# Kernel tuning notes

Measured on AMD Instinct MI355X. Metric: run time of the kernel, lower is better.

## Reference

```python
import jax, jax.numpy as jnp
import numpy as np

NUM_HEADS = 16


def setup_inputs() -> dict:
    key = jax.random.key(0)
    k1, k2, k3 = jax.random.split(key, 3)
    B, S, D = 2, 2048, 1024
    x = jax.random.normal(k1, (B, S, D), dtype=jnp.float32)
    # qkv_bias=False -> no bias on qkv projection; output Dense has default bias
    w_qkv = jax.random.normal(k2, (D, 3 * D), dtype=jnp.float32) * (1.0 / np.sqrt(D))
    w_out = jax.random.normal(k3, (D, D), dtype=jnp.float32) * (1.0 / np.sqrt(D))
    b_out = jnp.zeros((D,), dtype=jnp.float32)
    return {"x": x, "w_qkv": w_qkv, "w_out": w_out, "b_out": b_out}


def reference(x, w_qkv, w_out, b_out):
    B, S, D = x.shape
    H = NUM_HEADS
    Dh = D // H
    scale = 1.0 / np.sqrt(Dh).astype(np.float32)

    qkv = jnp.einsum('bsd,de->bse', x, w_qkv)           # [B,S,3D]
    q, k, v = jnp.split(qkv, 3, axis=-1)
    split = lambda t: t.reshape(B, S, H, Dh).transpose(0, 2, 1, 3)  # [B,H,S,Dh]
    q, k, v = split(q), split(k), split(v)

    attn = jnp.einsum('bhid,bhjd->bhij', q, k) * scale  # [B,H,S,S]
    # mask=None -> all-ones mask combined with causal mask => causal float mask
    causal = jnp.tril(jnp.ones((S, S), dtype=jnp.float32))[None, None]
    attn = causal * attn + (1.0 - causal) * (-1e9)
    attn = jax.nn.softmax(attn, axis=-1)

    out = jnp.einsum('bhij,bhjd->bhid', attn, v)        # [B,H,S,Dh]
    out = out.transpose(0, 2, 1, 3).reshape(B, S, D)    # merge heads
    return jnp.einsum('bsd,de->bse', out, w_out) + b_out
```

## Files before the change

### kernel.cpp

```cpp
#include <hip/hip_runtime.h>

typedef unsigned short u16;
typedef __bf16 bf16x8 __attribute__((ext_vector_type(8)));
typedef unsigned short u16x8 __attribute__((ext_vector_type(8)));
typedef float f32x4 __attribute__((ext_vector_type(4)));

union Frag { u16x8 u; bf16x8 b; };

__device__ __forceinline__ u16 f2bf(float f) {
  unsigned u = __builtin_bit_cast(unsigned, f);
  u += 0x7fff + ((u >> 16) & 1);
  return (u16)(u >> 16);
}

__device__ __forceinline__ f32x4 mfma16(bf16x8 a, bf16x8 b, f32x4 c) {
  return __builtin_amdgcn_mfma_f32_16x16x32_bf16(a, b, c, 0, 0, 0);
}

typedef const __attribute__((address_space(1))) void* as1cv;
typedef __attribute__((address_space(3))) void* as3v;

__device__ __forceinline__ void glds16(const u16* g, u16* l) {
  __builtin_amdgcn_global_load_lds((as1cv)g, (as3v)l, 16, 0, 0);
}

__global__ __launch_bounds__(256) void castf_bf(const float* __restrict__ src,
                                                u16* __restrict__ dst, int n4) {
  int i = blockIdx.x * blockDim.x + threadIdx.x;
  int stride = gridDim.x * blockDim.x;
  for (; i < n4; i += stride) {
    float4 v = ((const float4*)src)[i];
    ushort4 o;
    o.x = f2bf(v.x); o.y = f2bf(v.y); o.z = f2bf(v.z); o.w = f2bf(v.w);
    ((ushort4*)dst)[i] = o;
  }
}

__global__ __launch_bounds__(256) void cast_transpose(const float* __restrict__ src,
                                                      u16* __restrict__ dst, int K, int N) {
  __shared__ float tile[32][33];
  int tn = N >> 5;
  int bk = blockIdx.x / tn, bn = blockIdx.x % tn;
  int k0 = bk << 5, n0 = bn << 5;
  int tx = threadIdx.x, ty = threadIdx.y;
#pragma unroll
  for (int i = 0; i < 4; i++)
    tile[ty + 8 * i][tx] = src[(size_t)(k0 + ty + 8 * i) * N + n0 + tx];
  __syncthreads();
#pragma unroll
  for (int i = 0; i < 4; i++)
    dst[(size_t)(n0 + ty + 8 * i) * K + k0 + tx] = f2bf(tile[tx][ty + 8 * i]);
}

template <int FP32OUT>
__global__ __launch_bounds__(256) void gemm_bt(const u16* __restrict__ A,
                                               const u16* __restrict__ BT,
                                               void* __restrict__ Cout,
                                               const float* __restrict__ bias,
                                               int N, int K, int nbc) {
  __shared__ u16 Al[128 * 32];
  __shared__ u16 Bl[128 * 32];
  int bid = blockIdx.x;
  int br = bid / nbc, bc = bid % nbc;
  int tid = threadIdx.x;
  int w = tid >> 6, l = tid & 63;
  int lg = l >> 4, lq = l & 15;
  int wr = w >> 1, wc = w & 1;

  f32x4 acc[4][4];
#pragma unroll
  for (int m = 0; m < 4; m++)
#pragma unroll
    for (int n = 0; n < 4; n++)
      acc[m][n] = (f32x4){0.f, 0.f, 0.f, 0.f};

  const u16* Ab = A + (size_t)(br * 128 + 32 * w + (l >> 2)) * K + (l & 3) * 8;
  const u16* Bb = BT + (size_t)(bc * 128 + 32 * w + (l >> 2)) * K + (l & 3) * 8;
  u16* Ald = Al + 32 * w * 32;
  u16* Bld = Bl + 32 * w * 32;

  for (int kt = 0; kt < K; kt += 32) {
    glds16(Ab + kt, Ald);
    glds16(Ab + (size_t)16 * K + kt, Ald + 16 * 32);
    glds16(Bb + kt, Bld);
    glds16(Bb + (size_t)16 * K + kt, Bld + 16 * 32);
    __syncthreads();

    Frag af[4], bf[4];
#pragma unroll
    for (int m = 0; m < 4; m++)
      af[m].u = *(const u16x8*)(Al + (64 * wr + 16 * m + lq) * 32 + lg * 8);
#pragma unroll
    for (int n = 0; n < 4; n++)
      bf[n].u = *(const u16x8*)(Bl + (64 * wc + 16 * n + lq) * 32 + lg * 8);
#pragma unroll
    for (int m = 0; m < 4; m++)
#pragma unroll
      for (int n = 0; n < 4; n++)
        acc[m][n] = mfma16(af[m].b, bf[n].b, acc[m][n]);
    __syncthreads();
  }

  int row0 = br * 128 + 64 * wr + lg * 4;
  int col0 = bc * 128 + 64 * wc + lq;
  if (FP32OUT) {
    float* C = (float*)Cout;
#pragma unroll
    for (int n = 0; n < 4; n++) {
      float bv = bias[col0 + 16 * n];
#pragma unroll
      for (int m = 0; m < 4; m++)
#pragma unroll
        for (int r = 0; r < 4; r++)
          C[(size_t)(row0 + 16 * m + r) * N + col0 + 16 * n] = acc[m][n][r] + bv;
    }
  } else {
    u16* C = (u16*)Cout;
#pragma unroll
    for (int n = 0; n < 4; n++)
#pragma unroll
      for (int m = 0; m < 4; m++)
#pragma unroll
        for (int r = 0; r < 4; r++)
          C[(size_t)(row0 + 16 * m + r) * N + col0 + 16 * n] = f2bf(acc[m][n][r]);
  }
}

__global__ __launch_bounds__(256) void build_vt(const u16* __restrict__ qkv,
                                                u16* __restrict__ vt) {
  __shared__ u16 t[64][65];
  int bid = blockIdx.x;
  int s0 = (bid & 31) * 64;
  int bh = bid >> 5;
  int b = bh >> 4, h = bh & 15;
  int tid = threadIdx.x;
  int r = tid >> 2, c4 = (tid & 3) * 16;
  const u16* srow = qkv + (size_t)(b * 2048 + s0 + r) * 3072 + 2048 + h * 64 + c4;
  u16x8 v0 = *(const u16x8*)(srow);
  u16x8 v1 = *(const u16x8*)(srow + 8);
#pragma unroll
  for (int j = 0; j < 8; j++) { t[r][c4 + j] = v0[j]; t[r][c4 + 8 + j] = v1[j]; }
  __syncthreads();
  int dh = tid >> 2, sc = (tid & 3) * 16;
  u16 outv[16];
#pragma unroll
  for (int i = 0; i < 16; ++i) {
    int e = sc + i;
    int b32 = e >> 5, e32 = e & 31;
    int k = ((e32 >> 2) & 1) * 16 + (e32 >> 3) * 4 + (e32 & 3);
    outv[i] = t[b32 * 32 + k][dh];
  }
  u16* drow = vt + ((size_t)bh * 64 + dh) * 2048 + s0 + sc;
  *(u16x8*)drow = *(u16x8*)&outv[0];
  *(u16x8*)(drow + 8) = *(u16x8*)&outv[8];
}

__global__ __launch_bounds__(256) void flash_attn(const u16* __restrict__ qkv,
                                                  const u16* __restrict__ vt,
                                                  u16* __restrict__ aout) {
  __shared__ __align__(16) u16 pool[2][8192];
  const float SCALE = 0.125f;
  int bid = blockIdx.x;
  int qb = 31 - (bid >> 5);
  int bh = bid & 31;
  int b = bh >> 4, h = bh & 15;
  int tid = threadIdx.x;
  int w = tid >> 6, l = tid & 63;
  int lg = l >> 4, lq = l & 15;
  int q0w = qb * 64 + w * 16;
  int qidx = q0w + lq;

  const size_t rs = 3072;
  Frag qf0, qf1;
  const u16* qbase = qkv + (size_t)(b * 2048 + q0w + lq) * rs + h * 64 + lg * 8;
  qf0.u = *(const u16x8*)(qbase);
  qf1.u = *(const u16x8*)(qbase + 32);

  int srw = l >> 3;
  int scol = 8 * ((l & 7) ^ srw);
  const u16* kg = qkv + (size_t)(b * 2048) * rs + 1024 + h * 64;
  const u16* vg = vt + (size_t)bh * 64 * 2048;
  int r0 = (w * 2 + 0) * 8 + srw;
  int r1 = (w * 2 + 1) * 8 + srw;

  float m = -1e38f, lam = 0.f;
  f32x4 o[4];
#pragma unroll
  for (int d = 0; d < 4; ++d) o[d] = (f32x4){0.f, 0.f, 0.f, 0.f};
  int ntiles = qb + 1;

  glds16(kg + (size_t)r0 * rs + scol, &pool[0][(w * 2 + 0) * 512]);
  glds16(kg + (size_t)r1 * rs + scol, &pool[0][(w * 2 + 1) * 512]);
  glds16(vg + (size_t)r0 * 2048 + scol, &pool[0][4096 + (w * 2 + 0) * 512]);
  glds16(vg + (size_t)r1 * 2048 + scol, &pool[0][4096 + (w * 2 + 1) * 512]);
  __syncthreads();

  int swz = (lq & 7) << 3;
  for (int t = 0; t < ntiles; ++t) {
    int cur = t & 1;
    if (t + 1 < ntiles) {
      int kt2 = (t + 1) * 64;
      u16* nb = &pool[cur ^ 1][0];
      glds16(kg + (size_t)(kt2 + r0) * rs + scol, nb + (w * 2 + 0) * 512);
      glds16(kg + (size_t)(kt2 + r1) * rs + scol, nb + (w * 2 + 1) * 512);
      glds16(vg + (size_t)r0 * 2048 + kt2 + scol, nb + 4096 + (w * 2 + 0) * 512);
      glds16(vg + (size_t)r1 * 2048 + kt2 + scol, nb + 4096 + (w * 2 + 1) * 512);
    }
    int kt = t * 64;
    const u16* Kl = &pool[cur][0];
    const u16* Vl = &pool[cur][4096];

    f32x4 s[4];
#pragma unroll
    for (int sub = 0; sub < 4; ++sub) {
      int row = sub * 16 + lq;
      Frag k0, k1;
      k0.u = *(const u16x8*)(Kl + row * 64 + ((lg * 8) ^ swz));
      k1.u = *(const u16x8*)(Kl + row * 64 + ((32 + lg * 8) ^ swz));
      f32x4 z = {0.f, 0.f, 0.f, 0.f};
      s[sub] = mfma16(k0.b, qf0.b, z);
      s[sub] = mfma16(k1.b, qf1.b, s[sub]);
    }

    float tm = -1e38f;
    float sv[4][4];
    if (t == qb) {
#pragma unroll
      for (int sub = 0; sub < 4; ++sub)
#pragma unroll
        for (int r = 0; r < 4; ++r) {
          int key = kt + sub * 16 + lg * 4 + r;
          float v = s[sub][r] * SCALE;
          if (key > qidx) v = -1e30f;
          sv[sub][r] = v;
          tm = fmaxf(tm, v);
        }
    } else {
#pragma unroll
      for (int sub = 0; sub < 4; ++sub)
#pragma unroll
        for (int r = 0; r < 4; ++r) {
          float v = s[sub][r] * SCALE;
          sv[sub][r] = v;
          tm = fmaxf(tm, v);
        }
    }
    tm = fmaxf(tm, __shfl_xor(tm, 16));
    tm = fmaxf(tm, __shfl_xor(tm, 32));
    float mn = fmaxf(m, tm);
    float alpha = __expf(m - mn);
    float psum = 0.f;
    unsigned pp[4][2];
#pragma unroll
    for (int sub = 0; sub < 4; ++sub) {
#pragma unroll
      for (int tt = 0; tt < 2; ++tt) {
        float p0 = __expf(sv[sub][2 * tt] - mn);
        float p1 = __expf(sv[sub][2 * tt + 1] - mn);
        psum += p0 + p1;
        pp[sub][tt] = (unsigned)f2bf(p0) | ((unsigned)f2bf(p1) << 16);
      }
    }
    psum += __shfl_xor(psum, 16);
    psum += __shfl_xor(psum, 32);
    lam = lam * alpha + psum;
    m = mn;
#pragma unroll
    for (int d = 0; d < 4; ++d)
#pragma unroll
      for (int r = 0; r < 4; ++r) o[d][r] *= alpha;

#pragma unroll
    for (int hf = 0; hf < 2; ++hf) {
      union { unsigned w4[4]; u16x8 u; bf16x8 bv; } pf;
      pf.w4[0] = pp[2 * hf][0];
      pf.w4[1] = pp[2 * hf][1];
      pf.w4[2] = pp[2 * hf + 1][0];
      pf.w4[3] = pp[2 * hf + 1][1];
#pragma unroll
      for (int d = 0; d < 4; ++d) {
        int row = d * 16 + lq;
        Frag vf;
        vf.u = *(const u16x8*)(Vl + row * 64 + ((hf * 32 + lg * 8) ^ swz));
        o[d] = mfma16(vf.b, pf.bv, o[d]);
      }
    }
    __syncthreads();
  }

  float inv = 1.0f / lam;
  u16* Ost = &pool[0][0] + w * (16 * 72);
#pragma unroll
  for (int d = 0; d < 4; ++d)
#pragma unroll
    for (int r = 0; r < 4; ++r)
      Ost[lq * 72 + d * 16 + lg * 4 + r] = f2bf(o[d][r] * inv);
  int q = l >> 2, c16 = (l & 3) * 16;
  u16x8 t0, t1;
#pragma unroll
  for (int j = 0; j < 8; j++) { t0[j] = Ost[q * 72 + c16 + j]; t1[j] = Ost[q * 72 + c16 + 8 + j]; }
  u16* orow = aout + (size_t)(b * 2048 + qb * 64 + w * 16 + q) * 1024 + h * 64 + c16;
  *(u16x8*)orow = t0;
  *(u16x8*)(orow + 8) = t1;
}

extern "C" void kernel_launch(void* const* d_in, const int* in_sizes, int n_in,
                              void* d_out, int out_size, void* d_ws, size_t ws_size,
                              hipStream_t stream) {
  const float* x    = (const float*)d_in[0];
  const float* wqkv = (const float*)d_in[1];
  const float* wout = (const float*)d_in[2];
  const float* bout = (const float*)d_in[3];
  float* out = (float*)d_out;

  char* ws = (char*)d_ws;
  u16* xb    = (u16*)(ws);
  u16* wqkvT = (u16*)(ws + 8388608);
  u16* woutT = (u16*)(ws + 14680064);
  u16* qkvb  = (u16*)(ws + 16777216);
  u16* vtb   = (u16*)(ws + 41943040);
  u16* aoutb = (u16*)(ws + 50331648);

  castf_bf<<<1024, 256, 0, stream>>>(x, xb, (4096 * 1024) / 4);
  cast_transpose<<<(1024 / 32) * (3072 / 32), dim3(32, 8), 0, stream>>>(wqkv, wqkvT, 1024, 3072);
  cast_transpose<<<(1024 / 32) * (1024 / 32), dim3(32, 8), 0, stream>>>(wout, woutT, 1024, 1024);

  gemm_bt<0><<<(4096 / 128) * (3072 / 128), 256, 0, stream>>>(xb, wqkvT, qkvb, nullptr,
                                                              3072, 1024, 3072 / 128);
  build_vt<<<1024, 256, 0, stream>>>(qkvb, vtb);
  flash_attn<<<2 * 16 * (2048 / 64), 256, 0, stream>>>(qkvb, vtb, aoutb);

  gemm_bt<1><<<(4096 / 128) * (1024 / 128), 256, 0, stream>>>(aoutb, woutT, out, bout,
                                                              1024, 1024, 1024 / 128);
}
```

Measured before the change: 127.3 us.

## Pair causal query blocks per workgroup and process two key tiles per step

Flash attention now gives each workgroup two query blocks (qb and 31-qb), so causal work is balanced and the grid shrinks to 512 blocks. Each iteration loads and processes two K/V tiles at once with a four-buffer LDS pipeline. Softmax switches to raw exp2 with a pre-folded log2e scale, and output rescaling is skipped unless the running max grows by more than 8. MFMA sections also get s_setprio hints. These aim to cut imbalance, barrier count and exp cost, but double the LDS footprint, which may lower occupancy, and add register pressure.

Result: no change. 126.2 us (-0.9%).

```diff
diff --git a/kernel.cpp b/kernel.cpp
--- a/kernel.cpp
+++ b/kernel.cpp
@@ -15,6 +15,12 @@
 
 __device__ __forceinline__ f32x4 mfma16(bf16x8 a, bf16x8 b, f32x4 c) {
   return __builtin_amdgcn_mfma_f32_16x16x32_bf16(a, b, c, 0, 0, 0);
+}
+
+__device__ __forceinline__ float exp2_raw(float x) {
+  float r;
+  asm("v_exp_f32 %0, %1" : "=v"(r) : "v"(x));
+  return r;
 }
 
 typedef const __attribute__((address_space(1))) void* as1cv;
@@ -158,150 +164,193 @@
 __global__ __launch_bounds__(256) void flash_attn(const u16* __restrict__ qkv,
                                                   const u16* __restrict__ vt,
                                                   u16* __restrict__ aout) {
-  __shared__ __align__(16) u16 pool[2][8192];
-  const float SCALE = 0.125f;
+  __shared__ __align__(16) u16 pool[4][8192];
+  const float SL2E = 0.18033688011112043f;
   int bid = blockIdx.x;
-  int qb = 31 - (bid >> 5);
-  int bh = bid & 31;
+  int bh = bid >> 4;
+  int p = bid & 15;
   int b = bh >> 4, h = bh & 15;
   int tid = threadIdx.x;
   int w = tid >> 6, l = tid & 63;
   int lg = l >> 4, lq = l & 15;
-  int q0w = qb * 64 + w * 16;
-  int qidx = q0w + lq;
 
   const size_t rs = 3072;
-  Frag qf0, qf1;
-  const u16* qbase = qkv + (size_t)(b * 2048 + q0w + lq) * rs + h * 64 + lg * 8;
-  qf0.u = *(const u16x8*)(qbase);
-  qf1.u = *(const u16x8*)(qbase + 32);
-
   int srw = l >> 3;
   int scol = 8 * ((l & 7) ^ srw);
   const u16* kg = qkv + (size_t)(b * 2048) * rs + 1024 + h * 64;
   const u16* vg = vt + (size_t)bh * 64 * 2048;
   int r0 = (w * 2 + 0) * 8 + srw;
   int r1 = (w * 2 + 1) * 8 + srw;
-
-  float m = -1e38f, lam = 0.f;
-  f32x4 o[4];
-#pragma unroll
-  for (int d = 0; d < 4; ++d) o[d] = (f32x4){0.f, 0.f, 0.f, 0.f};
-  int ntiles = qb + 1;
-
-  glds16(kg + (size_t)r0 * rs + scol, &pool[0][(w * 2 + 0) * 512]);
-  glds16(kg + (size_t)r1 * rs + scol, &pool[0][(w * 2 + 1) * 512]);
-  glds16(vg + (size_t)r0 * 2048 + scol, &pool[0][4096 + (w * 2 + 0) * 512]);
-  glds16(vg + (size_t)r1 * 2048 + scol, &pool[0][4096 + (w * 2 + 1) * 512]);
-  __syncthreads();
-
   int swz = (lq & 7) << 3;
-  for (int t = 0; t < ntiles; ++t) {
-    int cur = t & 1;
-    if (t + 1 < ntiles) {
-      int kt2 = (t + 1) * 64;
-      u16* nb = &pool[cur ^ 1][0];
+
+  for (int seg = 0; seg < 2; ++seg) {
+    int qb = seg ? p : (31 - p);
+    int ntiles = qb + 1;
+    int q0w = qb * 64 + w * 16;
+    int qidx = q0w + lq;
+
+    if (seg) __syncthreads();
+
+    Frag qf0, qf1;
+    const u16* qbase = qkv + (size_t)(b * 2048 + q0w + lq) * rs + h * 64 + lg * 8;
+    qf0.u = *(const u16x8*)(qbase);
+    qf1.u = *(const u16x8*)(qbase + 32);
+
+    float m = -1e38f, lam = 0.f;
+    f32x4 o[4];
+#pragma unroll
+    for (int d = 0; d < 4; ++d) o[d] = (f32x4){0.f, 0.f, 0.f, 0.f};
+
+    auto stage = [&](int tile, int buf) {
+      int kt2 = tile * 64;
+      u16* nb = &pool[buf][0];
       glds16(kg + (size_t)(kt2 + r0) * rs + scol, nb + (w * 2 + 0) * 512);
       glds16(kg + (size_t)(kt2 + r1) * rs + scol, nb + (w * 2 + 1) * 512);
       glds16(vg + (size_t)r0 * 2048 + kt2 + scol, nb + 4096 + (w * 2 + 0) * 512);
       glds16(vg + (size_t)r1 * 2048 + kt2 + scol, nb + 4096 + (w * 2 + 1) * 512);
-    }
-    int kt = t * 64;
-    const u16* Kl = &pool[cur][0];
-    const u16* Vl = &pool[cur][4096];
-
-    f32x4 s[4];
-#pragma unroll
-    for (int sub = 0; sub < 4; ++sub) {
-      int row = sub * 16 + lq;
-      Frag k0, k1;
-      k0.u = *(const u16x8*)(Kl + row * 64 + ((lg * 8) ^ swz));
-      k1.u = *(const u16x8*)(Kl + row * 64 + ((32 + lg * 8) ^ swz));
-      f32x4 z = {0.f, 0.f, 0.f, 0.f};
-      s[sub] = mfma16(k0.b, qf0.b, z);
-      s[sub] = mfma16(k1.b, qf1.b, s[sub]);
-    }
-
-    float tm = -1e38f;
-    float sv[4][4];
-    if (t == qb) {
-#pragma unroll
-      for (int sub = 0; sub < 4; ++sub)
+    };
+
+    stage(0, 0);
+    if (ntiles > 1) stage(1, 1);
+    __syncthreads();
+
+    for (int t = 0; t < ntiles; t += 2) {
+      int pi = (t >> 1) & 1;
+      const u16* KlA = &pool[2 * pi][0];
+      const u16* VlA = &pool[2 * pi][4096];
+      const u16* KlB = &pool[2 * pi + 1][0];
+      const u16* VlB = &pool[2 * pi + 1][4096];
+      if (t + 2 < ntiles) stage(t + 2, 2 * (1 - pi));
+      if (t + 3 < ntiles) stage(t + 3, 2 * (1 - pi) + 1);
+      bool two = (t + 1 < ntiles);
+      int kt = t * 64;
+
+      f32x4 s[8];
+      __builtin_amdgcn_s_setprio(1);
+#pragma unroll
+      for (int sub = 0; sub < 4; ++sub) {
+        int row = sub * 16 + lq;
+        Frag k0, k1;
+        k0.u = *(const u16x8*)(KlA + row * 64 + ((lg * 8) ^ swz));
+        k1.u = *(const u16x8*)(KlA + row * 64 + ((32 + lg * 8) ^ swz));
+        f32x4 z = {0.f, 0.f, 0.f, 0.f};
+        s[sub] = mfma16(k0.b, qf0.b, z);
+        s[sub] = mfma16(k1.b, qf1.b, s[sub]);
+      }
+      if (two) {
+#pragma unroll
+        for (int sub = 0; sub < 4; ++sub) {
+          int row = sub * 16 + lq;
+          Frag k0, k1;
+          k0.u = *(const u16x8*)(KlB + row * 64 + ((lg * 8) ^ swz));
+          k1.u = *(const u16x8*)(KlB + row * 64 + ((32 + lg * 8) ^ swz));
+          f32x4 z = {0.f, 0.f, 0.f, 0.f};
+          s[4 + sub] = mfma16(k0.b, qf0.b, z);
+          s[4 + sub] = mfma16(k1.b, qf1.b, s[4 + sub]);
+        }
+      }
+      __builtin_amdgcn_s_setprio(0);
+
+      float sv[8][4];
+      float tm = -1e38f;
+      if (t + 2 >= ntiles) {
+#pragma unroll
+        for (int sub = 0; sub < 8; ++sub) {
+          if (sub >= 4 && !two) {
+#pragma unroll
+            for (int r = 0; r < 4; ++r) sv[sub][r] = -1e30f;
+            continue;
+          }
+#pragma unroll
+          for (int r = 0; r < 4; ++r) {
+            int key = kt + sub * 16 + lg * 4 + r;
+            float v = s[sub][r] * SL2E;
+            if (key > qidx) v = -1e30f;
+            sv[sub][r] = v;
+            tm = fmaxf(tm, v);
+          }
+        }
+      } else {
+#pragma unroll
+        for (int sub = 0; sub < 8; ++sub)
+#pragma unroll
+          for (int r = 0; r < 4; ++r) {
+            float v = s[sub][r] * SL2E;
+            sv[sub][r] = v;
+            tm = fmaxf(tm, v);
+          }
+      }
+      tm = fmaxf(tm, __shfl_xor(tm, 16));
+      tm = fmaxf(tm, __shfl_xor(tm, 32));
+
+      if (!__all(tm <= m + 8.0f)) {
+        float mn = fmaxf(m, tm);
+        float alpha = exp2_raw(m - mn);
+        lam *= alpha;
+#pragma unroll
+        for (int d = 0; d < 4; ++d)
+#pragma unroll
+          for (int r = 0; r < 4; ++r) o[d][r] *= alpha;
+        m = mn;
+      }
+
+      float psum = 0.f;
+      Frag pf[4];
+#pragma unroll
+      for (int hf = 0; hf < 4; ++hf) {
 #pragma unroll
         for (int r = 0; r < 4; ++r) {
-          int key = kt + sub * 16 + lg * 4 + r;
-          float v = s[sub][r] * SCALE;
-          if (key > qidx) v = -1e30f;
-          sv[sub][r] = v;
-          tm = fmaxf(tm, v);
+          float p0 = exp2_raw(sv[2 * hf][r] - m);
+          float p1 = exp2_raw(sv[2 * hf + 1][r] - m);
+          psum += p0 + p1;
+          pf[hf].b[r] = (__bf16)p0;
+          pf[hf].b[4 + r] = (__bf16)p1;
         }
-    } else {
-#pragma unroll
-      for (int sub = 0; sub < 4; ++sub)
-#pragma unroll
-        for (int r = 0; r < 4; ++r) {
-          float v = s[sub][r] * SCALE;
-          sv[sub][r] = v;
-          tm = fmaxf(tm, v);
-        }
-    }
-    tm = fmaxf(tm, __shfl_xor(tm, 16));
-    tm = fmaxf(tm, __shfl_xor(tm, 32));
-    float mn = fmaxf(m, tm);
-    float alpha = __expf(m - mn);
-    float psum = 0.f;
-    unsigned pp[4][2];
-#pragma unroll
-    for (int sub = 0; sub < 4; ++sub) {
-#pragma unroll
-      for (int tt = 0; tt < 2; ++tt) {
-        float p0 = __expf(sv[sub][2 * tt] - mn);
-        float p1 = __expf(sv[sub][2 * tt + 1] - mn);
-        psum += p0 + p1;
-        pp[sub][tt] = (unsigned)f2bf(p0) | ((unsigned)f2bf(p1) << 16);
-      }
-    }
-    psum += __shfl_xor(psum, 16);
-    psum += __shfl_xor(psum, 32);
-    lam = lam * alpha + psum;
-    m = mn;
-#pragma unroll
-    for (int d = 0; d < 4; ++d)
-#pragma unroll
-      for (int r = 0; r < 4; ++r) o[d][r] *= alpha;
-
-#pragma unroll
-    for (int hf = 0; hf < 2; ++hf) {
-      union { unsigned w4[4]; u16x8 u; bf16x8 bv; } pf;
-      pf.w4[0] = pp[2 * hf][0];
-      pf.w4[1] = pp[2 * hf][1];
-      pf.w4[2] = pp[2 * hf + 1][0];
-      pf.w4[3] = pp[2 * hf + 1][1];
+      }
+      psum += __shfl_xor(psum, 16);
+      psum += __shfl_xor(psum, 32);
+      lam += psum;
+
+      __builtin_amdgcn_s_setprio(1);
 #pragma unroll
       for (int d = 0; d < 4; ++d) {
         int row = d * 16 + lq;
-        Frag vf;
-        vf.u = *(const u16x8*)(Vl + row * 64 + ((hf * 32 + lg * 8) ^ swz));
-        o[d] = mfma16(vf.b, pf.bv, o[d]);
-      }
+        Frag vf0, vf1;
+        vf0.u = *(const u16x8*)(VlA + row * 64 + ((lg * 8) ^ swz));
+        vf1.u = *(const u16x8*)(VlA + row * 64 + ((32 + lg * 8) ^ swz));
+        o[d] = mfma16(vf0.b, pf[0].b, o[d]);
+        o[d] = mfma16(vf1.b, pf[1].b, o[d]);
+      }
+      if (two) {
+#pragma unroll
+        for (int d = 0; d < 4; ++d) {
+          int row = d * 16 + lq;
+          Frag vf0, vf1;
+          vf0.u = *(const u16x8*)(VlB + row * 64 + ((lg * 8) ^ swz));
+          vf1.u = *(const u16x8*)(VlB + row * 64 + ((32 + lg * 8) ^ swz));
+          o[d] = mfma16(vf0.b, pf[2].b, o[d]);
+          o[d] = mfma16(vf1.b, pf[3].b, o[d]);
+        }
+      }
+      __builtin_amdgcn_s_setprio(0);
+      __syncthreads();
     }
-    __syncthreads();
-  }
-
-  float inv = 1.0f / lam;
-  u16* Ost = &pool[0][0] + w * (16 * 72);
-#pragma unroll
-  for (int d = 0; d < 4; ++d)
-#pragma unroll
-    for (int r = 0; r < 4; ++r)
-      Ost[lq * 72 + d * 16 + lg * 4 + r] = f2bf(o[d][r] * inv);
-  int q = l >> 2, c16 = (l & 3) * 16;
-  u16x8 t0, t1;
-#pragma unroll
-  for (int j = 0; j < 8; j++) { t0[j] = Ost[q * 72 + c16 + j]; t1[j] = Ost[q * 72 + c16 + 8 + j]; }
-  u16* orow = aout + (size_t)(b * 2048 + qb * 64 + w * 16 + q) * 1024 + h * 64 + c16;
-  *(u16x8*)orow = t0;
-  *(u16x8*)(orow + 8) = t1;
+
+    float inv = 1.0f / lam;
+    u16* Ost = &pool[0][0] + w * (16 * 72);
+#pragma unroll
+    for (int d = 0; d < 4; ++d)
+#pragma unroll
+      for (int r = 0; r < 4; ++r)
+        Ost[lq * 72 + d * 16 + lg * 4 + r] = f2bf(o[d][r] * inv);
+    int q = l >> 2, c16 = (l & 3) * 16;
+    u16x8 t0, t1;
+#pragma unroll
+    for (int j = 0; j < 8; j++) { t0[j] = Ost[q * 72 + c16 + j]; t1[j] = Ost[q * 72 + c16 + 8 + j]; }
+    u16* orow = aout + (size_t)(b * 2048 + qb * 64 + w * 16 + q) * 1024 + h * 64 + c16;
+    *(u16x8*)orow = t0;
+    *(u16x8*)(orow + 8) = t1;
+  }
 }
 
 extern "C" void kernel_launch(void* const* d_in, const int* in_sizes, int n_in,
@@ -328,7 +377,7 @@
   gemm_bt<0><<<(4096 / 128) * (3072 / 128), 256, 0, stream>>>(xb, wqkvT, qkvb, nullptr,
                                                               3072, 1024, 3072 / 128);
   build_vt<<<1024, 256, 0, stream>>>(qkvb, vtb);
-  flash_attn<<<2 * 16 * (2048 / 64), 256, 0, stream>>>(qkvb, vtb, aoutb);
+  flash_attn<<<512, 256, 0, stream>>>(qkvb, vtb, aoutb);
 
   gemm_bt<1><<<(4096 / 128) * (1024 / 128), 256, 0, stream>>>(aoutb, woutT, out, bout,
                                                               1024, 1024, 1024 / 128);
```
